# Optimization experiments

Hardware: AMD Instinct MI355X
Metric: run time of the kernel (lower is better)

The kernel has to match this reference:

```python
import jax, jax.numpy as jnp
import numpy as np

N_MBED = 384
HEAD_SIZE = 64

def setup_inputs() -> dict:
    key = jax.random.key(0)
    kx, kq, kk, kv = jax.random.split(key, 4)
    B, T = 128, 256
    x = jax.random.normal(kx, (B, T, N_MBED), dtype=jnp.float32)
    # torch nn.Linear(n_mbed, head_size, bias=False): y = x @ W^T, W:[head_size, n_mbed].
    # We store the transposed weight [n_mbed, head_size] so y = x @ W.
    s = 1.0 / np.sqrt(N_MBED)
    Wq = jax.random.uniform(kq, (N_MBED, HEAD_SIZE), jnp.float32, -s, s)
    Wk = jax.random.uniform(kk, (N_MBED, HEAD_SIZE), jnp.float32, -s, s)
    Wv = jax.random.uniform(kv, (N_MBED, HEAD_SIZE), jnp.float32, -s, s)
    return {"x": x, "Wq": Wq, "Wk": Wk, "Wv": Wv}

def reference(x, Wq, Wk, Wv):
    B, T, C = x.shape  # C = n_mbed = 384
    q = x @ Wq  # [B,T,H]
    k = x @ Wk
    v = x @ Wv
    # Faithful to source: wei = k @ q^T, scaled by C**-0.5 (C = n_mbed, not head_size)
    wei = jnp.einsum('bth,bsh->bts', k, q) * (C ** -0.5)  # [B,T,T]
    mask = jnp.tril(jnp.ones((T, T), dtype=bool))
    wei = jnp.where(mask, wei, -jnp.inf)
    wei = jax.nn.softmax(wei, axis=-1)
    # dropout omitted (eval mode / identity)
    out = jnp.einsum('bts,bsh->bth', wei, v)  # [B,T,H]
    return out
```

## Files before the change

kernel.cpp:

```cpp
#include <hip/hip_runtime.h>
#include <hip/hip_bf16.h>
#include <math.h>

constexpr int kB = 128;
constexpr int kT = 256;
constexpr int kC = 384;
constexpr int kH = 64;

using bf16x8 = __attribute__((ext_vector_type(8))) short;
using f32x4  = __attribute__((ext_vector_type(4))) float;

union BF8 { bf16x8 v; __hip_bfloat162 h[4]; };
union BF4 { short4 s; __hip_bfloat162 h[2]; };

__device__ inline bf16x8 cvt8(float4 a, float4 b) {
    BF8 u;
    u.h[0] = __float22bfloat162_rn(float2{a.x, a.y});
    u.h[1] = __float22bfloat162_rn(float2{a.z, a.w});
    u.h[2] = __float22bfloat162_rn(float2{b.x, b.y});
    u.h[3] = __float22bfloat162_rn(float2{b.z, b.w});
    return u.v;
}
__device__ inline short4 cvt4(float4 a) {
    BF4 u;
    u.h[0] = __float22bfloat162_rn(float2{a.x, a.y});
    u.h[1] = __float22bfloat162_rn(float2{a.z, a.w});
    return u.s;
}
__device__ inline short bf1(float f) {
    __hip_bfloat16 h = __float2bfloat16(f);
    return *(short*)&h;
}

__global__ void prep_kernel(const float* __restrict__ Wq,
                            const float* __restrict__ Wk,
                            const float* __restrict__ Wv,
                            __hip_bfloat16* __restrict__ Wt) {
    int idx = blockIdx.x * 256 + threadIdx.x;
    int n = idx / kC, c = idx % kC;
    int w = n >> 6, h = n & 63;
    const float* W = (w == 0) ? Wq : (w == 1) ? Wk : Wv;
    float val = W[c * kH + h];
    if (w == 1) val *= 0.051031036307982884f;
    Wt[idx] = __float2bfloat16(val);
}

__global__ __launch_bounds__(512, 2) void fused_kernel(
    const float* __restrict__ x, const __hip_bfloat16* __restrict__ Wt,
    float* __restrict__ out)
{
    __shared__ short Qs[256 * 72];
    __shared__ short Ks[128 * 72];
    __shared__ short VTs[64 * 264];
    __shared__ short As[2][256 * 36];
    __shared__ short Bs[2][192 * 36];

    const int bid  = blockIdx.x;
    const int b    = ((bid >> 4) << 3) | (bid & 7);
    const int half = ((bid >> 3) & 1) ^ 1;
    const int t0   = half * 128;

    const int tid  = threadIdx.x;
    const int wave = tid >> 6, lane = tid & 63;
    const int m16  = lane & 15, quad = lane >> 4;
    const int wm = wave & 1, wn = wave >> 1;
    const short* wt = (const short*)Wt;
    const float* xb = x + (size_t)b * kT * kC;

    const bool mfmaAct = (half == 1) || (wm == 0);

    bool kskip[3];
#pragma unroll
    for (int j = 0; j < 3; ++j) {
        const int nt = wn * 3 + j;
        kskip[j] = (half == 1) && (wm == 0) && (nt >= 4) && (nt < 8);
    }

    const int arow = tid >> 1, acol = (tid & 1) * 16;
    const bool aAct = (half == 1) || (arow < 128);

    float4 la[4]; bf16x8 lb0, lb1;
    auto glod = [&](int k0) {
        if (aAct) {
#pragma unroll
            for (int i = 0; i < 4; ++i)
                la[i] = *(const float4*)(xb + (size_t)arow * kC + k0 + acol + 4 * i);
        }
        {
            int n = tid >> 2, kk = (tid & 3) * 8;
            lb0 = *(const bf16x8*)(wt + (size_t)n * kC + k0 + kk);
        }
        if (tid < 256) {
            int c = tid + 512;
            int n = c >> 2, kk = (c & 3) * 8;
            lb1 = *(const bf16x8*)(wt + (size_t)n * kC + k0 + kk);
        }
    };
    auto swr = [&](int d) {
        if (aAct) {
#pragma unroll
            for (int i = 0; i < 4; ++i)
                *(short4*)&As[d][arow * 36 + acol + 4 * i] = cvt4(la[i]);
        }
        {
            int n = tid >> 2, kk = (tid & 3) * 8;
            *(bf16x8*)&Bs[d][n * 36 + kk] = lb0;
        }
        if (tid < 256) {
            int c = tid + 512;
            int n = c >> 2, kk = (c & 3) * 8;
            *(bf16x8*)&Bs[d][n * 36 + kk] = lb1;
        }
    };

    f32x4 acc[8][3];
#pragma unroll
    for (int mt = 0; mt < 8; ++mt)
#pragma unroll
        for (int j = 0; j < 3; ++j) acc[mt][j] = f32x4{0.f, 0.f, 0.f, 0.f};

    glod(0);
    swr(0);
    __syncthreads();

    for (int s = 0; s < 12; ++s) {
        const int d = s & 1;
        if (s < 11) glod((s + 1) * 32);

        if (mfmaAct) {
            bf16x8 af[8];
#pragma unroll
            for (int mt = 0; mt < 8; ++mt)
                af[mt] = *(const bf16x8*)&As[d][(wm * 128 + mt * 16 + m16) * 36 + quad * 8];
#pragma unroll
            for (int j = 0; j < 3; ++j) {
                if (!kskip[j]) {
                    const bf16x8 bfr =
                        *(const bf16x8*)&Bs[d][((wn * 3 + j) * 16 + m16) * 36 + quad * 8];
#pragma unroll
                    for (int mt = 0; mt < 8; ++mt)
                        acc[mt][j] = __builtin_amdgcn_mfma_f32_16x16x32_bf16(
                            af[mt], bfr, acc[mt][j], 0, 0, 0);
                }
            }
        }

        if (s < 11) swr(d ^ 1);
        __syncthreads();
    }

    if (mfmaAct) {
#pragma unroll
        for (int mt = 0; mt < 8; ++mt) {
            const int mbase = wm * 128 + mt * 16 + quad * 4;
#pragma unroll
            for (int j = 0; j < 3; ++j) {
                const int nt = wn * 3 + j;
                const int w  = nt >> 2;
                const int h  = (nt & 3) * 16 + m16;
                if (w == 2) {
                    float4 f = make_float4(acc[mt][j][0], acc[mt][j][1],
                                           acc[mt][j][2], acc[mt][j][3]);
                    *(short4*)&VTs[h * 264 + mbase] = cvt4(f);
                } else if (w == 1) {
                    if ((mbase >> 7) == half) {
#pragma unroll
                        for (int r = 0; r < 4; ++r)
                            Ks[(mbase + r - t0) * 72 + h] = bf1(acc[mt][j][r]);
                    }
                } else {
#pragma unroll
                    for (int r = 0; r < 4; ++r)
                        Qs[(mbase + r) * 72 + h] = bf1(acc[mt][j][r]);
                }
            }
        }
    }
    __syncthreads();

    const int wband = t0 + wave * 16;
    float* Pw = (float*)(&As[0][0]) + wave * 16 * 68;

    const bf16x8 ka0 = *(const bf16x8*)&Ks[(wave * 16 + m16) * 72 + quad * 8];
    const bf16x8 ka1 = *(const bf16x8*)&Ks[(wave * 16 + m16) * 72 + quad * 8 + 32];

    f32x4 O[4];
    float m_[4], l_[4];
#pragma unroll
    for (int i = 0; i < 4; ++i) {
        O[i] = f32x4{0.f, 0.f, 0.f, 0.f};
        m_[i] = -INFINITY; l_[i] = 0.f;
    }

    const int ilast = wband >> 6;
    for (int i = 0; i <= ilast; ++i) {
        const bool diag = (i == ilast);
        const int jmax = diag ? (wave & 3) : 3;

        f32x4 S[4];
        const f32x4 Z = f32x4{0.f, 0.f, 0.f, 0.f};
#pragma unroll
        for (int j = 0; j < 4; ++j) {
            if (j <= jmax) {
                bf16x8 qb0 = *(const bf16x8*)&Qs[(i * 64 + j * 16 + m16) * 72 + quad * 8];
                bf16x8 qb1 = *(const bf16x8*)&Qs[(i * 64 + j * 16 + m16) * 72 + quad * 8 + 32];
                S[j] = __builtin_amdgcn_mfma_f32_16x16x32_bf16(ka0, qb0, Z, 0, 0, 0);
                S[j] = __builtin_amdgcn_mfma_f32_16x16x32_bf16(ka1, qb1, S[j], 0, 0, 0);
            }
        }
        if (diag) {
#pragma unroll
            for (int r = 0; r < 4; ++r)
                if (m16 > quad * 4 + r) S[jmax][r] = -INFINITY;
        }

        float P[4][4];
#pragma unroll
        for (int j = 0; j < 4; ++j)
#pragma unroll
            for (int r = 0; r < 4; ++r) P[j][r] = 0.f;
#pragma unroll
        for (int r = 0; r < 4; ++r) {
            float rm = -INFINITY;
#pragma unroll
            for (int j = 0; j < 4; ++j)
                if (j <= jmax) rm = fmaxf(rm, S[j][r]);
            rm = fmaxf(rm, __shfl_xor(rm, 1, 64));
            rm = fmaxf(rm, __shfl_xor(rm, 2, 64));
            rm = fmaxf(rm, __shfl_xor(rm, 4, 64));
            rm = fmaxf(rm, __shfl_xor(rm, 8, 64));
            const float mn = fmaxf(m_[r], rm);
            const float al = __expf(m_[r] - mn);
            m_[r] = mn;
            float rs = 0.f;
#pragma unroll
            for (int j = 0; j < 4; ++j) {
                if (j <= jmax) { P[j][r] = __expf(S[j][r] - mn); rs += P[j][r]; }
            }
            rs += __shfl_xor(rs, 1, 64);
            rs += __shfl_xor(rs, 2, 64);
            rs += __shfl_xor(rs, 4, 64);
            rs += __shfl_xor(rs, 8, 64);
            l_[r] = l_[r] * al + rs;
            O[0][r] *= al; O[1][r] *= al; O[2][r] *= al; O[3][r] *= al;
        }

#pragma unroll
        for (int j = 0; j < 4; ++j)
#pragma unroll
            for (int r = 0; r < 4; ++r)
                Pw[(quad * 4 + r) * 68 + j * 16 + m16] = P[j][r];
        const float* pr = Pw + m16 * 68 + quad * 8;
        bf16x8 pf0 = cvt8(*(const float4*)pr,        *(const float4*)(pr + 4));
        bf16x8 pf1 = cvt8(*(const float4*)(pr + 32), *(const float4*)(pr + 36));

#pragma unroll
        for (int ht = 0; ht < 4; ++ht) {
            bf16x8 vb0 = *(const bf16x8*)&VTs[(ht * 16 + m16) * 264 + i * 64 + quad * 8];
            bf16x8 vb1 = *(const bf16x8*)&VTs[(ht * 16 + m16) * 264 + i * 64 + quad * 8 + 32];
            O[ht] = __builtin_amdgcn_mfma_f32_16x16x32_bf16(pf0, vb0, O[ht], 0, 0, 0);
            O[ht] = __builtin_amdgcn_mfma_f32_16x16x32_bf16(pf1, vb1, O[ht], 0, 0, 0);
        }
    }

#pragma unroll
    for (int r = 0; r < 4; ++r) {
        const float inv = 1.f / l_[r];
        const size_t row = (size_t)(b * kT + wband + quad * 4 + r);
#pragma unroll
        for (int ht = 0; ht < 4; ++ht)
            out[row * kH + ht * 16 + m16] = O[ht][r] * inv;
    }
}

extern "C" void kernel_launch(void* const* d_in, const int* in_sizes, int n_in,
                              void* d_out, int out_size, void* d_ws, size_t ws_size,
                              hipStream_t stream) {
    const float* x  = (const float*)d_in[0];
    const float* Wq = (const float*)d_in[1];
    const float* Wk = (const float*)d_in[2];
    const float* Wv = (const float*)d_in[3];
    float* out = (float*)d_out;

    __hip_bfloat16* Wt = (__hip_bfloat16*)d_ws;

    prep_kernel<<<(192 * kC) / 256, 256, 0, stream>>>(Wq, Wk, Wv, Wt);
    fused_kernel<<<dim3(256), 512, 0, stream>>>(x, Wt, out);
}
```

Baseline: 111.7 us.

## Double block threads to 1024 with split-KV attention and merged softmax partials

Raises the workgroup from 512 to 1024 threads (16 waves). The projection GEMM is re-tiled so each wave covers 64 rows instead of 128, and the double-buffered loop is unrolled into explicit ping-pong buffers. In attention, two waves share each 16-row band and split the key blocks between them; their online-softmax partials are merged through shared memory before the output is written. P is now stored as bf16 in LDS rather than fp32, and the goal is more latency hiding per block, at the cost of extra merge syncs and more register pressure per thread.

```diff
diff --git a/kernel.cpp b/kernel.cpp
--- a/kernel.cpp
+++ b/kernel.cpp
@@ -45,15 +45,18 @@
     Wt[idx] = __float2bfloat16(val);
 }
 
-__global__ __launch_bounds__(512, 2) void fused_kernel(
+__global__ __launch_bounds__(1024, 4) void fused_kernel(
     const float* __restrict__ x, const __hip_bfloat16* __restrict__ Wt,
     float* __restrict__ out)
 {
-    __shared__ short Qs[256 * 72];
-    __shared__ short Ks[128 * 72];
-    __shared__ short VTs[64 * 264];
-    __shared__ short As[2][256 * 36];
-    __shared__ short Bs[2][192 * 36];
+    __shared__ __align__(16) short SM[76800];
+    short* Qs  = SM;
+    short* Ks  = SM + 18432;
+    short* VTs = SM + 27648;
+    short* As0 = SM + 44544;
+    short* As1 = SM + 53760;
+    short* Bs0 = SM + 62976;
+    short* Bs1 = SM + 69888;
 
     const int bid  = blockIdx.x;
     const int b    = ((bid >> 4) << 3) | (bid & 7);
@@ -63,96 +66,86 @@
     const int tid  = threadIdx.x;
     const int wave = tid >> 6, lane = tid & 63;
     const int m16  = lane & 15, quad = lane >> 4;
-    const int wm = wave & 1, wn = wave >> 1;
+    const int wm = wave & 3, wn = wave >> 2;
     const short* wt = (const short*)Wt;
     const float* xb = x + (size_t)b * kT * kC;
 
-    const bool mfmaAct = (half == 1) || (wm == 0);
+    const bool mfmaAct = (half == 1) || (wm < 2);
 
     bool kskip[3];
 #pragma unroll
     for (int j = 0; j < 3; ++j) {
         const int nt = wn * 3 + j;
-        kskip[j] = (half == 1) && (wm == 0) && (nt >= 4) && (nt < 8);
-    }
-
-    const int arow = tid >> 1, acol = (tid & 1) * 16;
+        kskip[j] = (half == 1) && (wm < 2) && (nt >= 4) && (nt < 8);
+    }
+
+    const int arow = tid >> 2, acol = (tid & 3) * 8;
     const bool aAct = (half == 1) || (arow < 128);
-
-    float4 la[4]; bf16x8 lb0, lb1;
-    auto glod = [&](int k0) {
+    const bool bAct = (tid < 768);
+
+    float4 la0[2], la1[2]; bf16x8 lb0, lb1;
+    auto glod = [&](float4* la, bf16x8& lb, int k0) {
         if (aAct) {
-#pragma unroll
-            for (int i = 0; i < 4; ++i)
-                la[i] = *(const float4*)(xb + (size_t)arow * kC + k0 + acol + 4 * i);
-        }
-        {
-            int n = tid >> 2, kk = (tid & 3) * 8;
-            lb0 = *(const bf16x8*)(wt + (size_t)n * kC + k0 + kk);
-        }
-        if (tid < 256) {
-            int c = tid + 512;
-            int n = c >> 2, kk = (c & 3) * 8;
-            lb1 = *(const bf16x8*)(wt + (size_t)n * kC + k0 + kk);
-        }
-    };
-    auto swr = [&](int d) {
+            la[0] = *(const float4*)(xb + (size_t)arow * kC + k0 + acol);
+            la[1] = *(const float4*)(xb + (size_t)arow * kC + k0 + acol + 4);
+        }
+        if (bAct)
+            lb = *(const bf16x8*)(wt + (size_t)(tid >> 2) * kC + k0 + (tid & 3) * 8);
+    };
+    auto swr = [&](short* Ad, short* Bd, const float4* la, const bf16x8& lb) {
         if (aAct) {
-#pragma unroll
-            for (int i = 0; i < 4; ++i)
-                *(short4*)&As[d][arow * 36 + acol + 4 * i] = cvt4(la[i]);
-        }
-        {
-            int n = tid >> 2, kk = (tid & 3) * 8;
-            *(bf16x8*)&Bs[d][n * 36 + kk] = lb0;
-        }
-        if (tid < 256) {
-            int c = tid + 512;
-            int n = c >> 2, kk = (c & 3) * 8;
-            *(bf16x8*)&Bs[d][n * 36 + kk] = lb1;
-        }
-    };
-
-    f32x4 acc[8][3];
-#pragma unroll
-    for (int mt = 0; mt < 8; ++mt)
+            *(short4*)&Ad[arow * 36 + acol]     = cvt4(la[0]);
+            *(short4*)&Ad[arow * 36 + acol + 4] = cvt4(la[1]);
+        }
+        if (bAct)
+            *(bf16x8*)&Bd[(tid >> 2) * 36 + (tid & 3) * 8] = lb;
+    };
+
+    f32x4 acc[4][3];
+#pragma unroll
+    for (int mt = 0; mt < 4; ++mt)
 #pragma unroll
         for (int j = 0; j < 3; ++j) acc[mt][j] = f32x4{0.f, 0.f, 0.f, 0.f};
 
-    glod(0);
-    swr(0);
-    __syncthreads();
-
-    for (int s = 0; s < 12; ++s) {
-        const int d = s & 1;
-        if (s < 11) glod((s + 1) * 32);
-
-        if (mfmaAct) {
-            bf16x8 af[8];
-#pragma unroll
-            for (int mt = 0; mt < 8; ++mt)
-                af[mt] = *(const bf16x8*)&As[d][(wm * 128 + mt * 16 + m16) * 36 + quad * 8];
-#pragma unroll
-            for (int j = 0; j < 3; ++j) {
-                if (!kskip[j]) {
-                    const bf16x8 bfr =
-                        *(const bf16x8*)&Bs[d][((wn * 3 + j) * 16 + m16) * 36 + quad * 8];
-#pragma unroll
-                    for (int mt = 0; mt < 8; ++mt)
-                        acc[mt][j] = __builtin_amdgcn_mfma_f32_16x16x32_bf16(
-                            af[mt], bfr, acc[mt][j], 0, 0, 0);
-                }
+    auto mstep = [&](const short* Ad, const short* Bd) {
+        if (!mfmaAct) return;
+        bf16x8 af[4];
+#pragma unroll
+        for (int mt = 0; mt < 4; ++mt)
+            af[mt] = *(const bf16x8*)&Ad[(wm * 64 + mt * 16 + m16) * 36 + quad * 8];
+#pragma unroll
+        for (int j = 0; j < 3; ++j) {
+            if (!kskip[j]) {
+                const bf16x8 bfr =
+                    *(const bf16x8*)&Bd[((wn * 3 + j) * 16 + m16) * 36 + quad * 8];
+#pragma unroll
+                for (int mt = 0; mt < 4; ++mt)
+                    acc[mt][j] = __builtin_amdgcn_mfma_f32_16x16x32_bf16(
+                        af[mt], bfr, acc[mt][j], 0, 0, 0);
             }
         }
-
-        if (s < 11) swr(d ^ 1);
+    };
+
+    glod(la0, lb0, 0);
+    glod(la1, lb1, 32);
+    swr(As0, Bs0, la0, lb0);
+    __syncthreads();
+
+    for (int s = 0; s < 12; s += 2) {
+        if (s < 10) glod(la0, lb0, (s + 2) * 32);
+        mstep(As0, Bs0);
+        swr(As1, Bs1, la1, lb1);
         __syncthreads();
+        if (s + 1 < 10) glod(la1, lb1, (s + 3) * 32);
+        mstep(As1, Bs1);
+        if (s + 1 < 11) swr(As0, Bs0, la0, lb0);
+        __syncthreads();
     }
 
     if (mfmaAct) {
 #pragma unroll
-        for (int mt = 0; mt < 8; ++mt) {
-            const int mbase = wm * 128 + mt * 16 + quad * 4;
+        for (int mt = 0; mt < 4; ++mt) {
+            const int mbase = wm * 64 + mt * 16 + quad * 4;
 #pragma unroll
             for (int j = 0; j < 3; ++j) {
                 const int nt = wn * 3 + j;
@@ -178,11 +171,13 @@
     }
     __syncthreads();
 
-    const int wband = t0 + wave * 16;
-    float* Pw = (float*)(&As[0][0]) + wave * 16 * 68;
-
-    const bf16x8 ka0 = *(const bf16x8*)&Ks[(wave * 16 + m16) * 72 + quad * 8];
-    const bf16x8 ka1 = *(const bf16x8*)&Ks[(wave * 16 + m16) * 72 + quad * 8 + 32];
+    const int band  = wave >> 1;
+    const int piece = wave & 1;
+    const int wband = t0 + band * 16;
+    short* Pb = As0 + wave * 1152;
+
+    const bf16x8 ka0 = *(const bf16x8*)&Ks[(band * 16 + m16) * 72 + quad * 8];
+    const bf16x8 ka1 = *(const bf16x8*)&Ks[(band * 16 + m16) * 72 + quad * 8 + 32];
 
     f32x4 O[4];
     float m_[4], l_[4];
@@ -193,9 +188,9 @@
     }
 
     const int ilast = wband >> 6;
-    for (int i = 0; i <= ilast; ++i) {
+    for (int i = piece; i <= ilast; i += 2) {
         const bool diag = (i == ilast);
-        const int jmax = diag ? (wave & 3) : 3;
+        const int jmax = diag ? (band & 3) : 3;
 
         f32x4 S[4];
         const f32x4 Z = f32x4{0.f, 0.f, 0.f, 0.f};
@@ -249,10 +244,9 @@
         for (int j = 0; j < 4; ++j)
 #pragma unroll
             for (int r = 0; r < 4; ++r)
-                Pw[(quad * 4 + r) * 68 + j * 16 + m16] = P[j][r];
-        const float* pr = Pw + m16 * 68 + quad * 8;
-        bf16x8 pf0 = cvt8(*(const float4*)pr,        *(const float4*)(pr + 4));
-        bf16x8 pf1 = cvt8(*(const float4*)(pr + 32), *(const float4*)(pr + 36));
+                Pb[(quad * 4 + r) * 72 + j * 16 + m16] = bf1(P[j][r]);
+        bf16x8 pf0 = *(const bf16x8*)&Pb[m16 * 72 + quad * 8];
+        bf16x8 pf1 = *(const bf16x8*)&Pb[m16 * 72 + quad * 8 + 32];
 
 #pragma unroll
         for (int ht = 0; ht < 4; ++ht) {
@@ -263,14 +257,39 @@
         }
     }
 
-#pragma unroll
-    for (int r = 0; r < 4; ++r) {
-        const float inv = 1.f / l_[r];
-        const size_t row = (size_t)(b * kT + wband + quad * 4 + r);
+    float* MB = (float*)Bs0;
+    auto mbWrite = [&](int slot) {
+        float* p = MB + ((size_t)slot * 64 + lane) * 25;
+#pragma unroll
+        for (int r = 0; r < 4; ++r) { p[r] = m_[r]; p[4 + r] = l_[r]; }
 #pragma unroll
         for (int ht = 0; ht < 4; ++ht)
-            out[row * kH + ht * 16 + m16] = O[ht][r] * inv;
-    }
+#pragma unroll
+            for (int r = 0; r < 4; ++r) p[8 + ht * 4 + r] = O[ht][r];
+    };
+    auto mergeOut = [&](int slot) {
+        const float* p = MB + ((size_t)slot * 64 + lane) * 25;
+#pragma unroll
+        for (int r = 0; r < 4; ++r) {
+            const float m1 = p[r], l1 = p[4 + r];
+            const float mn = fmaxf(m_[r], m1);
+            const float a0 = __expf(m_[r] - mn), a1 = __expf(m1 - mn);
+            const float linv = 1.f / (l_[r] * a0 + l1 * a1);
+            const size_t row = (size_t)(b * kT + wband + quad * 4 + r);
+#pragma unroll
+            for (int ht = 0; ht < 4; ++ht)
+                out[row * kH + ht * 16 + m16] =
+                    (O[ht][r] * a0 + p[8 + ht * 4 + r] * a1) * linv;
+        }
+    };
+
+    if (piece == 1 && band < 4) mbWrite(band);
+    __syncthreads();
+    if (piece == 0 && band < 4) mergeOut(band);
+    __syncthreads();
+    if (piece == 1 && band >= 4) mbWrite(band - 4);
+    __syncthreads();
+    if (piece == 0 && band >= 4) mergeOut(band - 4);
 }
 
 extern "C" void kernel_launch(void* const* d_in, const int* in_sizes, int n_in,
@@ -285,5 +304,5 @@
     __hip_bfloat16* Wt = (__hip_bfloat16*)d_ws;
 
     prep_kernel<<<(192 * kC) / 256, 256, 0, stream>>>(Wq, Wk, Wv, Wt);
-    fused_kernel<<<dim3(256), 512, 0, stream>>>(x, Wt, out);
-}
+    fused_kernel<<<dim3(256), 1024, 0, stream>>>(x, Wt, out);
+}
```

Measured after the change: 137.3 us. +22.9%, slower.

## Prefetch two stages ahead in projection GEMM and transpose S to simplify softmax

Applied to the files above, without the earlier changes.

The projection GEMM loop now keeps two register sets of global loads in flight, prefetching two K-steps ahead with an unrolled ping-pong so global latency is hidden better. In the attention loop, S is computed transposed (Q as the A operand), so each lane holds one query row. The row max and sum then need only two cross-quad shuffles instead of per-row four-step shuffles. P is converted to bf16 before it is written to LDS, which halves LDS traffic. MFMA sections are wrapped in s_setprio, at the cost of more registers and extra shuffles to broadcast the rescale factors.

```diff
diff --git a/kernel.cpp b/kernel.cpp
--- a/kernel.cpp
+++ b/kernel.cpp
@@ -10,17 +10,8 @@
 using bf16x8 = __attribute__((ext_vector_type(8))) short;
 using f32x4  = __attribute__((ext_vector_type(4))) float;
 
-union BF8 { bf16x8 v; __hip_bfloat162 h[4]; };
 union BF4 { short4 s; __hip_bfloat162 h[2]; };
 
-__device__ inline bf16x8 cvt8(float4 a, float4 b) {
-    BF8 u;
-    u.h[0] = __float22bfloat162_rn(float2{a.x, a.y});
-    u.h[1] = __float22bfloat162_rn(float2{a.z, a.w});
-    u.h[2] = __float22bfloat162_rn(float2{b.x, b.y});
-    u.h[3] = __float22bfloat162_rn(float2{b.z, b.w});
-    return u.v;
-}
 __device__ inline short4 cvt4(float4 a) {
     BF4 u;
     u.h[0] = __float22bfloat162_rn(float2{a.x, a.y});
@@ -79,8 +70,8 @@
     const int arow = tid >> 1, acol = (tid & 1) * 16;
     const bool aAct = (half == 1) || (arow < 128);
 
-    float4 la[4]; bf16x8 lb0, lb1;
-    auto glod = [&](int k0) {
+    float4 la0[4], la1[4]; bf16x8 lb0a, lb0b, lb1a, lb1b;
+    auto glod = [&](float4* la, bf16x8& lba, bf16x8& lbb, int k0) {
         if (aAct) {
 #pragma unroll
             for (int i = 0; i < 4; ++i)
@@ -88,15 +79,15 @@
         }
         {
             int n = tid >> 2, kk = (tid & 3) * 8;
-            lb0 = *(const bf16x8*)(wt + (size_t)n * kC + k0 + kk);
+            lba = *(const bf16x8*)(wt + (size_t)n * kC + k0 + kk);
         }
         if (tid < 256) {
             int c = tid + 512;
             int n = c >> 2, kk = (c & 3) * 8;
-            lb1 = *(const bf16x8*)(wt + (size_t)n * kC + k0 + kk);
+            lbb = *(const bf16x8*)(wt + (size_t)n * kC + k0 + kk);
         }
     };
-    auto swr = [&](int d) {
+    auto swr = [&](int d, const float4* la, const bf16x8& lba, const bf16x8& lbb) {
         if (aAct) {
 #pragma unroll
             for (int i = 0; i < 4; ++i)
@@ -104,12 +95,12 @@
         }
         {
             int n = tid >> 2, kk = (tid & 3) * 8;
-            *(bf16x8*)&Bs[d][n * 36 + kk] = lb0;
+            *(bf16x8*)&Bs[d][n * 36 + kk] = lba;
         }
         if (tid < 256) {
             int c = tid + 512;
             int n = c >> 2, kk = (c & 3) * 8;
-            *(bf16x8*)&Bs[d][n * 36 + kk] = lb1;
+            *(bf16x8*)&Bs[d][n * 36 + kk] = lbb;
         }
     };
 
@@ -119,33 +110,38 @@
 #pragma unroll
         for (int j = 0; j < 3; ++j) acc[mt][j] = f32x4{0.f, 0.f, 0.f, 0.f};
 
-    glod(0);
-    swr(0);
+    auto mstep = [&](int d) {
+        if (!mfmaAct) return;
+        bf16x8 af[8];
+#pragma unroll
+        for (int mt = 0; mt < 8; ++mt)
+            af[mt] = *(const bf16x8*)&As[d][(wm * 128 + mt * 16 + m16) * 36 + quad * 8];
+#pragma unroll
+        for (int j = 0; j < 3; ++j) {
+            if (!kskip[j]) {
+                const bf16x8 bfr =
+                    *(const bf16x8*)&Bs[d][((wn * 3 + j) * 16 + m16) * 36 + quad * 8];
+#pragma unroll
+                for (int mt = 0; mt < 8; ++mt)
+                    acc[mt][j] = __builtin_amdgcn_mfma_f32_16x16x32_bf16(
+                        af[mt], bfr, acc[mt][j], 0, 0, 0);
+            }
+        }
+    };
+
+    glod(la0, lb0a, lb0b, 0);
+    glod(la1, lb1a, lb1b, 32);
+    swr(0, la0, lb0a, lb0b);
     __syncthreads();
 
-    for (int s = 0; s < 12; ++s) {
-        const int d = s & 1;
-        if (s < 11) glod((s + 1) * 32);
-
-        if (mfmaAct) {
-            bf16x8 af[8];
-#pragma unroll
-            for (int mt = 0; mt < 8; ++mt)
-                af[mt] = *(const bf16x8*)&As[d][(wm * 128 + mt * 16 + m16) * 36 + quad * 8];
-#pragma unroll
-            for (int j = 0; j < 3; ++j) {
-                if (!kskip[j]) {
-                    const bf16x8 bfr =
-                        *(const bf16x8*)&Bs[d][((wn * 3 + j) * 16 + m16) * 36 + quad * 8];
-#pragma unroll
-                    for (int mt = 0; mt < 8; ++mt)
-                        acc[mt][j] = __builtin_amdgcn_mfma_f32_16x16x32_bf16(
-                            af[mt], bfr, acc[mt][j], 0, 0, 0);
-                }
-            }
-        }
-
-        if (s < 11) swr(d ^ 1);
+    for (int s = 0; s < 12; s += 2) {
+        if (s < 10) glod(la0, lb0a, lb0b, (s + 2) * 32);
+        mstep(0);
+        swr(1, la1, lb1a, lb1b);
+        __syncthreads();
+        if (s + 1 < 10) glod(la1, lb1a, lb1b, (s + 3) * 32);
+        mstep(1);
+        if (s + 1 < 11) swr(0, la0, lb0a, lb0b);
         __syncthreads();
     }
 
@@ -179,18 +175,15 @@
     __syncthreads();
 
     const int wband = t0 + wave * 16;
-    float* Pw = (float*)(&As[0][0]) + wave * 16 * 68;
+    short* Pb = &As[0][0] + wave * 1152;
 
     const bf16x8 ka0 = *(const bf16x8*)&Ks[(wave * 16 + m16) * 72 + quad * 8];
     const bf16x8 ka1 = *(const bf16x8*)&Ks[(wave * 16 + m16) * 72 + quad * 8 + 32];
 
     f32x4 O[4];
-    float m_[4], l_[4];
-#pragma unroll
-    for (int i = 0; i < 4; ++i) {
-        O[i] = f32x4{0.f, 0.f, 0.f, 0.f};
-        m_[i] = -INFINITY; l_[i] = 0.f;
-    }
+#pragma unroll
+    for (int i = 0; i < 4; ++i) O[i] = f32x4{0.f, 0.f, 0.f, 0.f};
+    float m_ = -INFINITY, l_ = 0.f;
 
     const int ilast = wband >> 6;
     for (int i = 0; i <= ilast; ++i) {
@@ -199,61 +192,78 @@
 
         f32x4 S[4];
         const f32x4 Z = f32x4{0.f, 0.f, 0.f, 0.f};
+        __builtin_amdgcn_s_setprio(1);
 #pragma unroll
         for (int j = 0; j < 4; ++j) {
             if (j <= jmax) {
-                bf16x8 qb0 = *(const bf16x8*)&Qs[(i * 64 + j * 16 + m16) * 72 + quad * 8];
-                bf16x8 qb1 = *(const bf16x8*)&Qs[(i * 64 + j * 16 + m16) * 72 + quad * 8 + 32];
-                S[j] = __builtin_amdgcn_mfma_f32_16x16x32_bf16(ka0, qb0, Z, 0, 0, 0);
-                S[j] = __builtin_amdgcn_mfma_f32_16x16x32_bf16(ka1, qb1, S[j], 0, 0, 0);
-            }
-        }
+                const int s = i * 64 + j * 16 + m16;
+                bf16x8 qb0 = *(const bf16x8*)&Qs[s * 72 + quad * 8];
+                bf16x8 qb1 = *(const bf16x8*)&Qs[s * 72 + quad * 8 + 32];
+                S[j] = __builtin_amdgcn_mfma_f32_16x16x32_bf16(qb0, ka0, Z, 0, 0, 0);
+                S[j] = __builtin_amdgcn_mfma_f32_16x16x32_bf16(qb1, ka1, S[j], 0, 0, 0);
+            }
+        }
+        __builtin_amdgcn_s_setprio(0);
         if (diag) {
 #pragma unroll
             for (int r = 0; r < 4; ++r)
-                if (m16 > quad * 4 + r) S[jmax][r] = -INFINITY;
-        }
+                if (quad * 4 + r > m16) S[jmax][r] = -INFINITY;
+        }
+
+        float rm = -INFINITY;
+#pragma unroll
+        for (int j = 0; j < 4; ++j)
+            if (j <= jmax)
+#pragma unroll
+                for (int r = 0; r < 4; ++r) rm = fmaxf(rm, S[j][r]);
+        rm = fmaxf(rm, __shfl_xor(rm, 16, 64));
+        rm = fmaxf(rm, __shfl_xor(rm, 32, 64));
+
+        const float mn = fmaxf(m_, rm);
+        const float al = __expf(m_ - mn);
+        m_ = mn;
 
         float P[4][4];
 #pragma unroll
         for (int j = 0; j < 4; ++j)
 #pragma unroll
             for (int r = 0; r < 4; ++r) P[j][r] = 0.f;
-#pragma unroll
-        for (int r = 0; r < 4; ++r) {
-            float rm = -INFINITY;
-#pragma unroll
-            for (int j = 0; j < 4; ++j)
-                if (j <= jmax) rm = fmaxf(rm, S[j][r]);
-            rm = fmaxf(rm, __shfl_xor(rm, 1, 64));
-            rm = fmaxf(rm, __shfl_xor(rm, 2, 64));
-            rm = fmaxf(rm, __shfl_xor(rm, 4, 64));
-            rm = fmaxf(rm, __shfl_xor(rm, 8, 64));
-            const float mn = fmaxf(m_[r], rm);
-            const float al = __expf(m_[r] - mn);
-            m_[r] = mn;
-            float rs = 0.f;
-#pragma unroll
-            for (int j = 0; j < 4; ++j) {
-                if (j <= jmax) { P[j][r] = __expf(S[j][r] - mn); rs += P[j][r]; }
-            }
-            rs += __shfl_xor(rs, 1, 64);
-            rs += __shfl_xor(rs, 2, 64);
-            rs += __shfl_xor(rs, 4, 64);
-            rs += __shfl_xor(rs, 8, 64);
-            l_[r] = l_[r] * al + rs;
-            O[0][r] *= al; O[1][r] *= al; O[2][r] *= al; O[3][r] *= al;
-        }
+        float rs = 0.f;
+#pragma unroll
+        for (int j = 0; j < 4; ++j) {
+            if (j <= jmax) {
+#pragma unroll
+                for (int r = 0; r < 4; ++r) {
+                    P[j][r] = __expf(S[j][r] - mn);
+                    rs += P[j][r];
+                }
+            }
+        }
+        rs += __shfl_xor(rs, 16, 64);
+        rs += __shfl_xor(rs, 32, 64);
+        l_ = l_ * al + rs;
+
+        float albc[4];
+#pragma unroll
+        for (int r = 0; r < 4; ++r)
+            albc[r] = __shfl(al, (quad << 4) | (quad * 4 + r), 64);
+#pragma unroll
+        for (int ht = 0; ht < 4; ++ht)
+#pragma unroll
+            for (int r = 0; r < 4; ++r) O[ht][r] *= albc[r];
 
 #pragma unroll
         for (int j = 0; j < 4; ++j)
 #pragma unroll
-            for (int r = 0; r < 4; ++r)
-                Pw[(quad * 4 + r) * 68 + j * 16 + m16] = P[j][r];
-        const float* pr = Pw + m16 * 68 + quad * 8;
-        bf16x8 pf0 = cvt8(*(const float4*)pr,        *(const float4*)(pr + 4));
-        bf16x8 pf1 = cvt8(*(const float4*)(pr + 32), *(const float4*)(pr + 36));
-
+            for (int p = 0; p < 2; ++p) {
+                __hip_bfloat162 w =
+                    __float22bfloat162_rn(float2{P[j][2 * p], P[j][2 * p + 1]});
+                *(__hip_bfloat162*)&Pb[m16 * 72 + j * 16 + quad * 4 + 2 * p] = w;
+            }
+        bf16x8 pf0 = *(const bf16x8*)&Pb[m16 * 72 + quad * 8];
+        bf16x8 pf1 = *(const bf16x8*)&Pb[m16 * 72 + quad * 8 + 32];
+
+        __builtin_amdgcn_s_setprio(1);
 #pragma unroll
         for (int ht = 0; ht < 4; ++ht) {
             bf16x8 vb0 = *(const bf16x8*)&VTs[(ht * 16 + m16) * 264 + i * 64 + quad * 8];
@@ -261,11 +271,16 @@
             O[ht] = __builtin_amdgcn_mfma_f32_16x16x32_bf16(pf0, vb0, O[ht], 0, 0, 0);
             O[ht] = __builtin_amdgcn_mfma_f32_16x16x32_bf16(pf1, vb1, O[ht], 0, 0, 0);
         }
-    }
-
+        __builtin_amdgcn_s_setprio(0);
+    }
+
+    float lbc[4];
+#pragma unroll
+    for (int r = 0; r < 4; ++r)
+        lbc[r] = __shfl(l_, (quad << 4) | (quad * 4 + r), 64);
 #pragma unroll
     for (int r = 0; r < 4; ++r) {
-        const float inv = 1.f / l_[r];
+        const float inv = 1.f / lbc[r];
         const size_t row = (size_t)(b * kT + wband + quad * 4 + r);
 #pragma unroll
         for (int ht = 0; ht < 4; ++ht)
```

Result: slower. 114.4 us (+2.4%).
